# Kernel optimization log

Hardware: AMD Instinct MI355X
Metric: run time of the kernel (lower is better)

Reference implementation:

```python
import jax, jax.numpy as jnp
import numpy as np
from jax import lax
from jax.scipy.special import ndtr

EV = 6           # even context kernel size
K = 3            # num_mixtures
GROUPS = 3       # grouped 1x1 convs (grps=3 for clrchs<3)
SCALE_MIN = 0.11 # lower bound on mixture std
LP = 257         # 257 CDF sampling points (8-bit Y/RGB path)


def _cdf_pts():
    # cdf_sampling_pts__Y_RGB from __init__
    pts = jnp.linspace(-127.5, 128.5, LP) / 255.0
    pts = pts.at[0].set(-147.5 / 255.0).at[-1].set(148.5 / 255.0)
    return pts.astype(jnp.float32)


def _conv(x, w, b, groups=1):
    y = lax.conv_general_dilated(
        x, w, window_strides=(1, 1), padding='VALID',
        dimension_numbers=('NCHW', 'OIHW', 'NCHW'),
        feature_group_count=groups)
    return y + b[None, :, None, None]


def _forward_float(y_condition, W0, b0, W1, b1, W2, b2):
    # replicate pad: paddd0_00_11 = (Ev//2-1, Ev//2, Ev//2-1, Ev//2)
    y = jnp.pad(y_condition, ((0, 0), (0, 0), (EV // 2 - 1, EV // 2), (EV // 2 - 1, EV // 2)), mode='edge')
    h = jax.nn.relu(_conv(y, W0, b0, groups=1))        # [B, 192, H, W]
    h = jax.nn.relu(_conv(h, W1, b1, groups=GROUPS))   # [B, 192, H, W]
    p = _conv(h, W2, b2, groups=GROUPS)                # [B, 9, H, W] GMM params
    B, _, H, W = p.shape
    p = p.reshape(B, 3, K, H, W)                       # param-major: mu / raw_scale / raw_weight
    mu, sr, wr = p[:, 0], p[:, 1], p[:, 2]             # each [B, K, H, W]
    scale = jnp.maximum(jnp.exp(sr), SCALE_MIN)
    wts = jax.nn.softmax(wr, axis=1)                   # mixture weights over K
    t = _cdf_pts()                                     # [LP]
    z = (t - mu[..., None]) / scale[..., None]         # [B, K, H, W, LP]
    cdf = jnp.einsum('bkhw,bkhwl->bhwl', wts, ndtr(z)) # mixture CDF, [B, H, W, LP]
    return jnp.clip(cdf, 0.0, 1.0 - 1e-6)


def setup_inputs() -> dict:
    key = jax.random.key(0)
    ks = jax.random.split(key, 4)
    return {
        'y_condition': jax.random.uniform(ks[0], (1, 1, 256, 256), jnp.float32),
        'W0': jax.random.normal(ks[1], (192, 1, EV, EV), jnp.float32) * 0.05,
        'b0': jnp.zeros((192,), jnp.float32),
        'W1': jax.random.normal(ks[2], (192, 64, 1, 1), jnp.float32) * 0.05,
        'b1': jnp.zeros((192,), jnp.float32),
        'W2': jax.random.normal(ks[3], (9, 64, 1, 1), jnp.float32) * 0.05,
        'b2': jnp.zeros((9,), jnp.float32),
    }


def reference(y_condition, W0, b0, W1, b1, W2, b2):
    cdf_f = _forward_float(y_condition, W0, b0, W1, b1, W2, b2)
    # _convert_to_int_and_normalize with needs_normalization=True
    new_max = jnp.float32(2 ** 16 - (LP - 1))
    cdf_i = jnp.round(cdf_f * new_max).astype(jnp.int16)
    cdf_i = cdf_i + jnp.arange(LP, dtype=jnp.int16)
    return cdf_i
```

## Files before the change

### kernel.cpp

```cpp
#include <hip/hip_runtime.h>
#include <math.h>

#define LPTS 257
#define NPIX 65536
#define PPB  32
#define W1T_LD 68


__device__ __forceinline__ float xla_exp32(float x)
{
#pragma clang fp contract(off)
    x = fminf(x, 88.3762626647950f);
    x = fmaxf(x, -87.3365478515625f);
    const float m = floorf(fmaf(x, 1.44269504088896341f, 0.5f));
    float r = fmaf(m, -0.693359375f, x);
    r = fmaf(m, 2.12194440e-4f, r);
    const float r2 = r * r;
    float p = 1.9875691500e-4f;
    p = fmaf(p, r, 1.3981999507e-3f);
    p = fmaf(p, r, 8.3334519073e-3f);
    p = fmaf(p, r, 4.1665795894e-2f);
    p = fmaf(p, r, 1.6666665459e-1f);
    p = fmaf(p, r, 5.0000001201e-1f);
    float y = fmaf(p, r2, r) + 1.0f;
    const int e = (int)m;
    const float s = __int_as_float((e + 127) << 23);
    return y * s;
}

__device__ __forceinline__ float ieee_div(float n, float d)
{
    const float r0 = __builtin_amdgcn_rcpf(d);
    const float e  = fmaf(-d, r0, 1.0f);
    const float r1 = fmaf(e, r0, r0);
    const float q0 = n * r1;
    const float e1 = fmaf(-d, q0, n);
    const float q1 = fmaf(e1, r1, q0);
    const float e2 = fmaf(-d, q1, n);
    return fmaf(e2, r1, q1);
}

__device__ __forceinline__ float xla_erf32(float x)
{
#pragma clang fp contract(off)
    x = fminf(fmaxf(x, -4.0f), 4.0f);
    const float x2 = x * x;
    float pa = -2.72614225801306e-10f;
    pa = fmaf(pa, x2, 2.77068142495902e-08f);
    pa = fmaf(pa, x2, -2.10102402082508e-06f);
    pa = fmaf(pa, x2, -5.69250639462346e-05f);
    pa = fmaf(pa, x2, -7.34990630326855e-04f);
    pa = fmaf(pa, x2, -2.95459980854025e-03f);
    pa = fmaf(pa, x2, -1.60960333262415e-02f);
    float pb = -1.45660718464996e-05f;
    pb = fmaf(pb, x2, -2.13374055278905e-04f);
    pb = fmaf(pb, x2, -1.68282697438203e-03f);
    pb = fmaf(pb, x2, -7.37332916720468e-03f);
    pb = fmaf(pb, x2, -1.42647390514189e-02f);
    return ieee_div(x * pa, pb);
}

__device__ __forceinline__ float xla_erfc_ge1(float x)
{
#pragma clang fp contract(off)
    const float z = xla_exp32(-(x * x));
    const float q = 1.0f / x;
    const float y2 = q * q;
    float p;
    if (x < 2.0f) {
        p = 2.326819970068386e-02f;
        p = fmaf(p, y2, -1.387039388740657e-01f);
        p = fmaf(p, y2, 3.687424674597105e-01f);
        p = fmaf(p, y2, -5.824733027278666e-01f);
        p = fmaf(p, y2, 6.210004621745983e-01f);
        p = fmaf(p, y2, -4.944515323274145e-01f);
        p = fmaf(p, y2, 3.404879937665872e-01f);
        p = fmaf(p, y2, -2.741127028184656e-01f);
        p = fmaf(p, y2, 5.638259427386472e-01f);
    } else {
        p = -1.047766399936249e+01f;
        p = fmaf(p, y2, 1.297719955372516e+01f);
        p = fmaf(p, y2, -7.495518717768503e+00f);
        p = fmaf(p, y2, 2.921019019210786e+00f);
        p = fmaf(p, y2, -1.015265279202700e+00f);
        p = fmaf(p, y2, 4.218463358204948e-01f);
        p = fmaf(p, y2, -2.820767439740514e-01f);
        p = fmaf(p, y2, 5.641895067754075e-01f);
    }
    return z * q * p;
}

__device__ __forceinline__ void xla_ndtr3_y(
    float z0, float z1, float z2, float& o0, float& o1, float& o2)
{
#pragma clang fp contract(off)
    const float c = __uint_as_float(0x3f3504f3u);
    const float w0 = z0 * c, w1 = z1 * c, w2 = z2 * c;
    const float a0 = fabsf(w0), a1 = fabsf(w1), a2 = fabsf(w2);

    const float E0 = xla_erf32(w0);
    const float E1 = xla_erf32(w1);
    const float E2 = xla_erf32(w2);

    const float m0 = 1.0f - fabsf(E0);
    const float m1 = 1.0f - fabsf(E1);
    const float m2 = 1.0f - fabsf(E2);

    float y0 = (a0 < c) ? (1.0f + E0) : ((w0 > 0.0f) ? (2.0f - m0) : m0);
    float y1 = (a1 < c) ? (1.0f + E1) : ((w1 > 0.0f) ? (2.0f - m1) : m1);
    float y2 = (a2 < c) ? (1.0f + E2) : ((w2 > 0.0f) ? (2.0f - m2) : m2);

    const float amax = fmaxf(fmaxf(a0, a1), a2);
    if (__builtin_expect(__ballot(amax > 1.0f) != 0ull, 0)) {
        {
            const float ec = xla_erfc_ge1(a0);
            const float yc = (w0 > 0.0f) ? (2.0f - ec) : ec;
            y0 = (a0 > 1.0f) ? yc : y0;
        }
        {
            const float ec = xla_erfc_ge1(a1);
            const float yc = (w1 > 0.0f) ? (2.0f - ec) : ec;
            y1 = (a1 > 1.0f) ? yc : y1;
        }
        {
            const float ec = xla_erfc_ge1(a2);
            const float yc = (w2 > 0.0f) ? (2.0f - ec) : ec;
            y2 = (a2 > 1.0f) ? yc : y2;
        }
    }
    o0 = y0; o1 = y1; o2 = y2;
}

__device__ __forceinline__ float xla_ndtr32(float zf)
{
#pragma clang fp contract(off)
    const float c = __uint_as_float(0x3f3504f3u);
    const float w = zf * c;
    const float aw = fabsf(w);
    const float E = xla_erf32(w);
    const float e_mid = 1.0f - fabsf(E);
    float y = (aw < c) ? (1.0f + E)
                       : ((w > 0.0f) ? (2.0f - e_mid) : e_mid);
    if (__builtin_expect(__ballot(aw > 1.0f) != 0ull, 0)) {
        const float ec = xla_erfc_ge1(aw);
        const float yc = (w > 0.0f) ? (2.0f - ec) : ec;
        y = (aw > 1.0f) ? yc : y;
    }
    return 0.5f * y;
}

__device__ __forceinline__ int quantize(float cdf, int l)
{
    int r = (int)rintf(cdf * 65280.0f);
    r = r > 32767 ? 32767 : r;
    r = r < -32768 ? -32768 : r;
    return (int)((short)(r + l));
}

__global__ __launch_bounds__(256, 1) void entropy_params(
    const float* __restrict__ y,
    const float* __restrict__ W0, const float* __restrict__ b0,
    const float* __restrict__ W1, const float* __restrict__ b1,
    const float* __restrict__ W2, const float* __restrict__ b2,
    float* __restrict__ prm_g)
{
#pragma clang fp contract(off)
    __shared__ float tile[21][22];
    __shared__ __align__(16) float w0s[64 * 36];
    __shared__ __align__(16) float w1t[64 * W1T_LD];
    __shared__ __align__(16) float w2t[64 * 4];
    __shared__ __align__(16) float b0s[64];
    __shared__ __align__(16) float b1s[64];
    __shared__ float b2s[3];

    const int bx  = blockIdx.x & 15;
    const int by  = blockIdx.x >> 4;
    const int g   = blockIdx.y;
    const int tid = threadIdx.x;
    const int tx  = tid & 15;
    const int ty  = tid >> 4;

    {
        const float4* src = (const float4*)(W0 + g * 64 * 36);
        for (int i = tid; i < 576; i += 256) ((float4*)w0s)[i] = src[i];
    }
    {
        const float4* src = (const float4*)(W1 + g * 4096);
        for (int i4 = tid; i4 < 1024; i4 += 256) {
            const float4 v = src[i4];
            const int c2 = i4 >> 4;
            const int c1 = (i4 << 2) & 63;
            w1t[(c1 + 0) * W1T_LD + c2] = v.x;
            w1t[(c1 + 1) * W1T_LD + c2] = v.y;
            w1t[(c1 + 2) * W1T_LD + c2] = v.z;
            w1t[(c1 + 3) * W1T_LD + c2] = v.w;
        }
    }
    if (tid < 64) {
        const int c2 = tid;
        w2t[c2 * 4 + 0] = W2[(3 * g + 0) * 64 + c2];
        w2t[c2 * 4 + 1] = W2[(3 * g + 1) * 64 + c2];
        w2t[c2 * 4 + 2] = W2[(3 * g + 2) * 64 + c2];
        w2t[c2 * 4 + 3] = 0.0f;
    }
    {
        const float4* s0 = (const float4*)(b0 + g * 64);
        const float4* s1 = (const float4*)(b1 + g * 64);
        if (tid < 16)      ((float4*)b0s)[tid]      = s0[tid];
        else if (tid < 32) ((float4*)b1s)[tid - 16] = s1[tid - 16];
        if (tid < 3) b2s[tid] = b2[3 * g + tid];
    }
    for (int idx = tid; idx < 21 * 21; idx += 256) {
        const int r = idx / 21;
        const int c = idx - r * 21;
        int gy = by * 16 - 2 + r; gy = gy < 0 ? 0 : (gy > 255 ? 255 : gy);
        int gx = bx * 16 - 2 + c; gx = gx < 0 ? 0 : (gx > 255 ? 255 : gx);
        tile[r][c] = y[gy * 256 + gx];
    }
    __syncthreads();

    float patch[36];
#pragma unroll
    for (int i = 0; i < 6; ++i)
#pragma unroll
        for (int j = 0; j < 6; ++j)
            patch[i * 6 + j] = tile[ty + i][tx + j];

    float acc2[64];
#pragma unroll
    for (int j = 0; j < 64; ++j) acc2[j] = 0.0f;

#pragma unroll 2
    for (int c1 = 0; c1 < 64; ++c1) {
        const float4* w4 = (const float4*)(w0s + c1 * 36);
        float h = 0.0f;
#pragma unroll
        for (int q = 0; q < 9; ++q) {
            const float4 wv = w4[q];
            h = fmaf(wv.x, patch[4 * q + 0], h);
            h = fmaf(wv.y, patch[4 * q + 1], h);
            h = fmaf(wv.z, patch[4 * q + 2], h);
            h = fmaf(wv.w, patch[4 * q + 3], h);
        }
        h = fmaxf(h + b0s[c1], 0.0f);

        const float4* w1r = (const float4*)(w1t + c1 * W1T_LD);
#pragma unroll
        for (int qq = 0; qq < 16; ++qq) {
            const float4 wv = w1r[qq];
            acc2[4 * qq + 0] = fmaf(wv.x, h, acc2[4 * qq + 0]);
            acc2[4 * qq + 1] = fmaf(wv.y, h, acc2[4 * qq + 1]);
            acc2[4 * qq + 2] = fmaf(wv.z, h, acc2[4 * qq + 2]);
            acc2[4 * qq + 3] = fmaf(wv.w, h, acc2[4 * qq + 3]);
        }
    }

    float p0 = 0.0f, p1 = 0.0f, p2 = 0.0f;
#pragma unroll
    for (int c2 = 0; c2 < 64; ++c2) {
        const float h1 = fmaxf(acc2[c2] + b1s[c2], 0.0f);
        const float4 wv = *(const float4*)(w2t + c2 * 4);
        p0 = fmaf(wv.x, h1, p0);
        p1 = fmaf(wv.y, h1, p1);
        p2 = fmaf(wv.z, h1, p2);
    }
    p0 += b2s[0]; p1 += b2s[1]; p2 += b2s[2];

    const int pix = (by * 16 + ty) * 256 + bx * 16 + tx;

    if (g == 0) {
        prm_g[0 * NPIX + pix] = p0;
        prm_g[1 * NPIX + pix] = p1;
        prm_g[2 * NPIX + pix] = p2;
    } else if (g == 1) {
        const float s0 = fmaxf(xla_exp32(p0), 0.11f);
        const float s1 = fmaxf(xla_exp32(p1), 0.11f);
        const float s2 = fmaxf(xla_exp32(p2), 0.11f);
        prm_g[3 * NPIX + pix] = s0;
        prm_g[4 * NPIX + pix] = s1;
        prm_g[5 * NPIX + pix] = s2;
        prm_g[6 * NPIX + pix] = 1.0f / s0;
        prm_g[7 * NPIX + pix] = 1.0f / s1;
        prm_g[8 * NPIX + pix] = 1.0f / s2;
    } else {
        const float m  = fmaxf(fmaxf(p0, p1), p2);
        const float e0 = xla_exp32(p0 - m);
        const float e1 = xla_exp32(p1 - m);
        const float e2 = xla_exp32(p2 - m);
        const float s  = (e0 + e1) + e2;
        prm_g[ 9 * NPIX + pix] = 0.5f * (e0 / s);
        prm_g[10 * NPIX + pix] = 0.5f * (e1 / s);
        prm_g[11 * NPIX + pix] = 0.5f * (e2 / s);
    }
}

__global__ __launch_bounds__(256) void entropy_cdf(
    const float* __restrict__ prm_g,
    int* __restrict__ out)
{
#pragma clang fp contract(off)
    __shared__ __align__(16) float prm[PPB][12];

    const int base = blockIdx.x * PPB;
    const int tid  = threadIdx.x;

    for (int i = tid; i < 12 * PPB; i += 256) {
        const int j = i >> 5;
        const int p = i & 31;
        prm[p][j] = prm_g[j * NPIX + base + p];
    }
    __syncthreads();

    const float CLIP = (float)(1.0 - 1e-6);

    {
        const int l = tid;
        const float t32 = (l == 0)
            ? (float)(-147.5 / 255.0)
            : (float)((((double)l) - 127.5) / 255.0);
#pragma unroll 4
        for (int p = 0; p < PPB; ++p) {
            const float4 v0 = *(const float4*)&prm[p][0];
            const float4 v1 = *(const float4*)&prm[p][4];
            const float4 v2 = *(const float4*)&prm[p][8];

            const float x0 = t32 - v0.x;
            const float x1 = t32 - v0.y;
            const float x2 = t32 - v0.z;
            const float qa = x0 * v1.z;
            const float qb = x1 * v1.w;
            const float qc = x2 * v2.x;
            const float ra = fmaf(-v0.w, qa, x0);
            const float rb = fmaf(-v1.x, qb, x1);
            const float rc = fmaf(-v1.y, qc, x2);
            const float z0 = fmaf(ra, v1.z, qa);
            const float z1 = fmaf(rb, v1.w, qb);
            const float z2 = fmaf(rc, v2.x, qc);

            float y0, y1, y2;
            xla_ndtr3_y(z0, z1, z2, y0, y1, y2);

            float cdf = fmaf(v2.w, y2, fmaf(v2.z, y1, v2.y * y0));
            cdf = fminf(fmaxf(cdf, 0.0f), CLIP);

            out[(size_t)(base + p) * LPTS + l] = quantize(cdf, l);
        }
    }

    if (tid < PPB) {
        const int p = tid;
        const float t32 = (float)(148.5 / 255.0);
        const float4 v0 = *(const float4*)&prm[p][0];
        const float4 v1 = *(const float4*)&prm[p][4];
        const float4 v2 = *(const float4*)&prm[p][8];

        const float x0 = t32 - v0.x;
        const float x1 = t32 - v0.y;
        const float x2 = t32 - v0.z;
        const float qa = x0 * v1.z;
        const float qb = x1 * v1.w;
        const float qc = x2 * v2.x;
        const float ra = fmaf(-v0.w, qa, x0);
        const float rb = fmaf(-v1.x, qb, x1);
        const float rc = fmaf(-v1.y, qc, x2);
        const float z0 = fmaf(ra, v1.z, qa);
        const float z1 = fmaf(rb, v1.w, qb);
        const float z2 = fmaf(rc, v2.x, qc);

        float y0, y1, y2;
        xla_ndtr3_y(z0, z1, z2, y0, y1, y2);

        float cdf = fmaf(v2.w, y2, fmaf(v2.z, y1, v2.y * y0));
        cdf = fminf(fmaxf(cdf, 0.0f), CLIP);

        out[(size_t)(base + p) * LPTS + 256] = quantize(cdf, 256);
    }
}

__global__ __launch_bounds__(256) void entropy_fused(
    const float* __restrict__ y,
    const float* __restrict__ W0, const float* __restrict__ b0,
    const float* __restrict__ W1, const float* __restrict__ b1,
    const float* __restrict__ W2, const float* __restrict__ b2,
    int* __restrict__ out)
{
#pragma clang fp contract(off)

    __shared__ float tile[21][22];
    __shared__ float prm[9][257];

    const int bx  = blockIdx.x & 15;
    const int by  = blockIdx.x >> 4;
    const int tid = threadIdx.x;
    const int tx  = tid & 15;
    const int ty  = tid >> 4;

    for (int idx = tid; idx < 21 * 21; idx += 256) {
        const int r = idx / 21;
        const int c = idx - r * 21;
        int gy = by * 16 - 2 + r; gy = gy < 0 ? 0 : (gy > 255 ? 255 : gy);
        int gx = bx * 16 - 2 + c; gx = gx < 0 ? 0 : (gx > 255 ? 255 : gx);
        tile[r][c] = y[gy * 256 + gx];
    }
    __syncthreads();

    float patch[36];
#pragma unroll
    for (int i = 0; i < 6; ++i)
#pragma unroll
        for (int j = 0; j < 6; ++j)
            patch[i * 6 + j] = tile[ty + i][tx + j];

    for (int g = 0; g < 3; ++g) {
        float h0[64];
#pragma unroll
        for (int c = 0; c < 64; ++c) {
            float acc = 0.0f;
            const float* w = W0 + (g * 64 + c) * 36;
#pragma unroll
            for (int k = 0; k < 36; ++k)
                acc = fmaf(w[k], patch[k], acc);
            acc = acc + b0[g * 64 + c];
            h0[c] = fmaxf(acc, 0.0f);
        }

        float p0 = 0.0f, p1 = 0.0f, p2 = 0.0f;
#pragma unroll 2
        for (int c = 0; c < 64; ++c) {
            float acc = 0.0f;
            const float* w = W1 + (g * 64 + c) * 64;
#pragma unroll
            for (int j = 0; j < 64; ++j)
                acc = fmaf(w[j], h0[j], acc);
            acc = acc + b1[g * 64 + c];
            acc = fmaxf(acc, 0.0f);
            p0 = fmaf(W2[(3 * g + 0) * 64 + c], acc, p0);
            p1 = fmaf(W2[(3 * g + 1) * 64 + c], acc, p1);
            p2 = fmaf(W2[(3 * g + 2) * 64 + c], acc, p2);
        }
        p0 = p0 + b2[3 * g + 0];
        p1 = p1 + b2[3 * g + 1];
        p2 = p2 + b2[3 * g + 2];

        if (g == 0) {
            prm[0][tid] = p0; prm[1][tid] = p1; prm[2][tid] = p2;
        } else if (g == 1) {
            prm[3][tid] = fmaxf(xla_exp32(p0), 0.11f);
            prm[4][tid] = fmaxf(xla_exp32(p1), 0.11f);
            prm[5][tid] = fmaxf(xla_exp32(p2), 0.11f);
        } else {
            const float m  = fmaxf(fmaxf(p0, p1), p2);
            const float e0 = xla_exp32(p0 - m);
            const float e1 = xla_exp32(p1 - m);
            const float e2 = xla_exp32(p2 - m);
            const float s  = (e0 + e1) + e2;
            prm[6][tid] = e0 / s;
            prm[7][tid] = e1 / s;
            prm[8][tid] = e2 / s;
        }
    }
    __syncthreads();

    const int rowbase = (by * 16) * 256 + bx * 16;
    const float CLIP = (float)(1.0 - 1e-6);

    {
        const int l = tid;
        const float t32 = (l == 0)
            ? (float)(-147.5 / 255.0)
            : (float)((((double)l) - 127.5) / 255.0);
        for (int p = 0; p < 256; ++p) {
            const float mu0 = prm[0][p], mu1 = prm[1][p], mu2 = prm[2][p];
            const float sc0 = prm[3][p], sc1 = prm[4][p], sc2 = prm[5][p];
            const float w0  = prm[6][p], w1  = prm[7][p], w2  = prm[8][p];

            const float n0 = xla_ndtr32((t32 - mu0) / sc0);
            const float n1 = xla_ndtr32((t32 - mu1) / sc1);
            const float n2 = xla_ndtr32((t32 - mu2) / sc2);

            float cdf = fmaf(w2, n2, fmaf(w1, n1, w0 * n0));
            cdf = fminf(fmaxf(cdf, 0.0f), CLIP);

            const int pix = rowbase + (p >> 4) * 256 + (p & 15);
            out[(size_t)pix * LPTS + l] = quantize(cdf, l);
        }
    }

    {
        const int p = tid;
        const float t32 = (float)(148.5 / 255.0);
        const float mu0 = prm[0][p], mu1 = prm[1][p], mu2 = prm[2][p];
        const float sc0 = prm[3][p], sc1 = prm[4][p], sc2 = prm[5][p];
        const float w0  = prm[6][p], w1  = prm[7][p], w2  = prm[8][p];

        const float n0 = xla_ndtr32((t32 - mu0) / sc0);
        const float n1 = xla_ndtr32((t32 - mu1) / sc1);
        const float n2 = xla_ndtr32((t32 - mu2) / sc2);

        float cdf = fmaf(w2, n2, fmaf(w1, n1, w0 * n0));
        cdf = fminf(fmaxf(cdf, 0.0f), CLIP);

        const int pix = rowbase + (p >> 4) * 256 + (p & 15);
        out[(size_t)pix * LPTS + 256] = quantize(cdf, 256);
    }
}

extern "C" void kernel_launch(void* const* d_in, const int* in_sizes, int n_in,
                              void* d_out, int out_size, void* d_ws, size_t ws_size,
                              hipStream_t stream)
{
    const float* y  = (const float*)d_in[0];
    const float* W0 = (const float*)d_in[1];
    const float* b0 = (const float*)d_in[2];
    const float* W1 = (const float*)d_in[3];
    const float* b1 = (const float*)d_in[4];
    const float* W2 = (const float*)d_in[5];
    const float* b2 = (const float*)d_in[6];

    int* out = (int*)d_out;

    const size_t need = (size_t)12 * NPIX * sizeof(float);
    if (d_ws != nullptr && ws_size >= need) {
        float* prm_g = (float*)d_ws;
        entropy_params<<<dim3(256, 3), dim3(256), 0, stream>>>(
            y, W0, b0, W1, b1, W2, b2, prm_g);
        entropy_cdf<<<dim3(NPIX / PPB), dim3(256), 0, stream>>>(prm_g, out);
    } else {
        entropy_fused<<<dim3(256), dim3(256), 0, stream>>>(
            y, W0, b0, W1, b1, W2, b2, out);
    }
}
```

Before: 175.1 us.

## Split per-pixel channel work across four threads with shared-memory staging

The params kernel now gives each pixel four threads instead of one. Each thread computes 16 of the 64 channels for the conv0 and grouped conv1 stages, and the intermediate activations are staged in shared memory between stages. The block tile shrinks to 8x8 pixels, the grid grows fourfold, and the single-block occupancy hint is dropped. This cuts per-thread register pressure (the 64-float accumulator array is gone) and raises parallelism, at the cost of extra LDS traffic, three more barriers, and a final 9-output projection done by only one thread per pixel.

Result: slower. 180.2 us (+3.0%).

```diff
diff --git a/kernel.cpp b/kernel.cpp
--- a/kernel.cpp
+++ b/kernel.cpp
@@ -4,7 +4,7 @@
 #define LPTS 257
 #define NPIX 65536
 #define PPB  32
-#define W1T_LD 68
+#define SW   68
 
 
 __device__ __forceinline__ float xla_exp32(float x)
@@ -157,7 +157,7 @@
     return (int)((short)(r + l));
 }
 
-__global__ __launch_bounds__(256, 1) void entropy_params(
+__global__ __launch_bounds__(256) void entropy_params(
     const float* __restrict__ y,
     const float* __restrict__ W0, const float* __restrict__ b0,
     const float* __restrict__ W1, const float* __restrict__ b1,
@@ -165,23 +165,26 @@
     float* __restrict__ prm_g)
 {
 #pragma clang fp contract(off)
-    __shared__ float tile[21][22];
+    __shared__ __align__(16) float tile[13][16];
     __shared__ __align__(16) float w0s[64 * 36];
-    __shared__ __align__(16) float w1t[64 * W1T_LD];
+    __shared__ __align__(16) float w1s[64 * SW];
     __shared__ __align__(16) float w2t[64 * 4];
     __shared__ __align__(16) float b0s[64];
     __shared__ __align__(16) float b1s[64];
     __shared__ float b2s[3];
-
-    const int bx  = blockIdx.x & 15;
-    const int by  = blockIdx.x >> 4;
+    __shared__ __align__(16) float h0s[64 * SW];
+
+    const int bx  = blockIdx.x & 31;
+    const int by  = blockIdx.x >> 5;
     const int g   = blockIdx.y;
     const int tid = threadIdx.x;
-    const int tx  = tid & 15;
-    const int ty  = tid >> 4;
+    const int p   = tid >> 2;
+    const int t   = tid & 3;
+    const int py  = p >> 3;
+    const int px  = p & 7;
 
     {
-        const float4* src = (const float4*)(W0 + g * 64 * 36);
+        const float4* src = (const float4*)(W0 + g * 2304);
         for (int i = tid; i < 576; i += 256) ((float4*)w0s)[i] = src[i];
     }
     {
@@ -189,33 +192,28 @@
         for (int i4 = tid; i4 < 1024; i4 += 256) {
             const float4 v = src[i4];
             const int c2 = i4 >> 4;
-            const int c1 = (i4 << 2) & 63;
-            w1t[(c1 + 0) * W1T_LD + c2] = v.x;
-            w1t[(c1 + 1) * W1T_LD + c2] = v.y;
-            w1t[(c1 + 2) * W1T_LD + c2] = v.z;
-            w1t[(c1 + 3) * W1T_LD + c2] = v.w;
+            const int k4 = (i4 & 15) << 2;
+            *(float4*)&w1s[c2 * SW + k4] = v;
         }
     }
     if (tid < 64) {
-        const int c2 = tid;
-        w2t[c2 * 4 + 0] = W2[(3 * g + 0) * 64 + c2];
-        w2t[c2 * 4 + 1] = W2[(3 * g + 1) * 64 + c2];
-        w2t[c2 * 4 + 2] = W2[(3 * g + 2) * 64 + c2];
-        w2t[c2 * 4 + 3] = 0.0f;
-    }
-    {
-        const float4* s0 = (const float4*)(b0 + g * 64);
-        const float4* s1 = (const float4*)(b1 + g * 64);
-        if (tid < 16)      ((float4*)b0s)[tid]      = s0[tid];
-        else if (tid < 32) ((float4*)b1s)[tid - 16] = s1[tid - 16];
-        if (tid < 3) b2s[tid] = b2[3 * g + tid];
-    }
-    for (int idx = tid; idx < 21 * 21; idx += 256) {
-        const int r = idx / 21;
-        const int c = idx - r * 21;
-        int gy = by * 16 - 2 + r; gy = gy < 0 ? 0 : (gy > 255 ? 255 : gy);
-        int gx = bx * 16 - 2 + c; gx = gx < 0 ? 0 : (gx > 255 ? 255 : gx);
-        tile[r][c] = y[gy * 256 + gx];
+        w2t[tid * 4 + 0] = W2[(3 * g + 0) * 64 + tid];
+        w2t[tid * 4 + 1] = W2[(3 * g + 1) * 64 + tid];
+        w2t[tid * 4 + 2] = W2[(3 * g + 2) * 64 + tid];
+        w2t[tid * 4 + 3] = 0.0f;
+    } else if (tid < 128) {
+        b0s[tid - 64] = b0[g * 64 + (tid - 64)];
+    } else if (tid < 192) {
+        b1s[tid - 128] = b1[g * 64 + (tid - 128)];
+    }
+    if (tid < 3) b2s[tid] = b2[3 * g + tid];
+
+    if (tid < 169) {
+        const int rr = tid / 13;
+        const int cc = tid - rr * 13;
+        int gy = by * 8 - 2 + rr;  gy = gy < 0 ? 0 : (gy > 255 ? 255 : gy);
+        int gx = bx * 8 - 2 + cc;  gx = gx < 0 ? 0 : (gx > 255 ? 255 : gx);
+        tile[rr][cc] = y[gy * 256 + gx];
     }
     __syncthreads();
 
@@ -224,73 +222,100 @@
     for (int i = 0; i < 6; ++i)
 #pragma unroll
         for (int j = 0; j < 6; ++j)
-            patch[i * 6 + j] = tile[ty + i][tx + j];
-
-    float acc2[64];
-#pragma unroll
-    for (int j = 0; j < 64; ++j) acc2[j] = 0.0f;
-
-#pragma unroll 2
-    for (int c1 = 0; c1 < 64; ++c1) {
-        const float4* w4 = (const float4*)(w0s + c1 * 36);
-        float h = 0.0f;
-#pragma unroll
-        for (int q = 0; q < 9; ++q) {
-            const float4 wv = w4[q];
-            h = fmaf(wv.x, patch[4 * q + 0], h);
-            h = fmaf(wv.y, patch[4 * q + 1], h);
-            h = fmaf(wv.z, patch[4 * q + 2], h);
-            h = fmaf(wv.w, patch[4 * q + 3], h);
-        }
-        h = fmaxf(h + b0s[c1], 0.0f);
-
-        const float4* w1r = (const float4*)(w1t + c1 * W1T_LD);
-#pragma unroll
-        for (int qq = 0; qq < 16; ++qq) {
-            const float4 wv = w1r[qq];
-            acc2[4 * qq + 0] = fmaf(wv.x, h, acc2[4 * qq + 0]);
-            acc2[4 * qq + 1] = fmaf(wv.y, h, acc2[4 * qq + 1]);
-            acc2[4 * qq + 2] = fmaf(wv.z, h, acc2[4 * qq + 2]);
-            acc2[4 * qq + 3] = fmaf(wv.w, h, acc2[4 * qq + 3]);
-        }
-    }
-
-    float p0 = 0.0f, p1 = 0.0f, p2 = 0.0f;
-#pragma unroll
-    for (int c2 = 0; c2 < 64; ++c2) {
-        const float h1 = fmaxf(acc2[c2] + b1s[c2], 0.0f);
-        const float4 wv = *(const float4*)(w2t + c2 * 4);
-        p0 = fmaf(wv.x, h1, p0);
-        p1 = fmaf(wv.y, h1, p1);
-        p2 = fmaf(wv.z, h1, p2);
-    }
-    p0 += b2s[0]; p1 += b2s[1]; p2 += b2s[2];
-
-    const int pix = (by * 16 + ty) * 256 + bx * 16 + tx;
-
-    if (g == 0) {
-        prm_g[0 * NPIX + pix] = p0;
-        prm_g[1 * NPIX + pix] = p1;
-        prm_g[2 * NPIX + pix] = p2;
-    } else if (g == 1) {
-        const float s0 = fmaxf(xla_exp32(p0), 0.11f);
-        const float s1 = fmaxf(xla_exp32(p1), 0.11f);
-        const float s2 = fmaxf(xla_exp32(p2), 0.11f);
-        prm_g[3 * NPIX + pix] = s0;
-        prm_g[4 * NPIX + pix] = s1;
-        prm_g[5 * NPIX + pix] = s2;
-        prm_g[6 * NPIX + pix] = 1.0f / s0;
-        prm_g[7 * NPIX + pix] = 1.0f / s1;
-        prm_g[8 * NPIX + pix] = 1.0f / s2;
-    } else {
-        const float m  = fmaxf(fmaxf(p0, p1), p2);
-        const float e0 = xla_exp32(p0 - m);
-        const float e1 = xla_exp32(p1 - m);
-        const float e2 = xla_exp32(p2 - m);
-        const float s  = (e0 + e1) + e2;
-        prm_g[ 9 * NPIX + pix] = 0.5f * (e0 / s);
-        prm_g[10 * NPIX + pix] = 0.5f * (e1 / s);
-        prm_g[11 * NPIX + pix] = 0.5f * (e2 / s);
+            patch[i * 6 + j] = tile[py + i][px + j];
+
+    float h[16];
+#pragma unroll
+    for (int j = 0; j < 16; ++j) h[j] = 0.0f;
+#pragma unroll
+    for (int q = 0; q < 9; ++q) {
+        const float pk0 = patch[4 * q + 0];
+        const float pk1 = patch[4 * q + 1];
+        const float pk2 = patch[4 * q + 2];
+        const float pk3 = patch[4 * q + 3];
+#pragma unroll
+        for (int j = 0; j < 16; ++j) {
+            const int c1 = t + 4 * j;
+            const float4 wv = *(const float4*)&w0s[c1 * 36 + 4 * q];
+            h[j] = fmaf(wv.x, pk0, h[j]);
+            h[j] = fmaf(wv.y, pk1, h[j]);
+            h[j] = fmaf(wv.z, pk2, h[j]);
+            h[j] = fmaf(wv.w, pk3, h[j]);
+        }
+    }
+#pragma unroll
+    for (int j = 0; j < 16; ++j) {
+        const int c1 = t + 4 * j;
+        h0s[p * SW + c1] = fmaxf(h[j] + b0s[c1], 0.0f);
+    }
+    __syncthreads();
+
+    float a2[16];
+#pragma unroll
+    for (int j = 0; j < 16; ++j) a2[j] = 0.0f;
+#pragma unroll
+    for (int k = 0; k < 16; ++k) {
+        const float4 hv = *(const float4*)&h0s[p * SW + 4 * k];
+#pragma unroll
+        for (int j = 0; j < 16; ++j) {
+            const int c2 = t + 4 * j;
+            const float4 wv = *(const float4*)&w1s[c2 * SW + 4 * k];
+            a2[j] = fmaf(wv.x, hv.x, a2[j]);
+            a2[j] = fmaf(wv.y, hv.y, a2[j]);
+            a2[j] = fmaf(wv.z, hv.z, a2[j]);
+            a2[j] = fmaf(wv.w, hv.w, a2[j]);
+        }
+    }
+    __syncthreads();
+#pragma unroll
+    for (int j = 0; j < 16; ++j) {
+        const int c2 = t + 4 * j;
+        h0s[p * SW + c2] = fmaxf(a2[j] + b1s[c2], 0.0f);
+    }
+    __syncthreads();
+
+    if (t == 0) {
+        float p0 = 0.0f, p1 = 0.0f, p2 = 0.0f;
+#pragma unroll
+        for (int k = 0; k < 16; ++k) {
+            const float4 hv = *(const float4*)&h0s[p * SW + 4 * k];
+            const float hva[4] = {hv.x, hv.y, hv.z, hv.w};
+#pragma unroll
+            for (int i = 0; i < 4; ++i) {
+                const float4 wv = *(const float4*)&w2t[(4 * k + i) * 4];
+                p0 = fmaf(wv.x, hva[i], p0);
+                p1 = fmaf(wv.y, hva[i], p1);
+                p2 = fmaf(wv.z, hva[i], p2);
+            }
+        }
+        p0 += b2s[0]; p1 += b2s[1]; p2 += b2s[2];
+
+        const int pix = (by * 8 + py) * 256 + bx * 8 + px;
+
+        if (g == 0) {
+            prm_g[0 * NPIX + pix] = p0;
+            prm_g[1 * NPIX + pix] = p1;
+            prm_g[2 * NPIX + pix] = p2;
+        } else if (g == 1) {
+            const float s0 = fmaxf(xla_exp32(p0), 0.11f);
+            const float s1 = fmaxf(xla_exp32(p1), 0.11f);
+            const float s2 = fmaxf(xla_exp32(p2), 0.11f);
+            prm_g[3 * NPIX + pix] = s0;
+            prm_g[4 * NPIX + pix] = s1;
+            prm_g[5 * NPIX + pix] = s2;
+            prm_g[6 * NPIX + pix] = 1.0f / s0;
+            prm_g[7 * NPIX + pix] = 1.0f / s1;
+            prm_g[8 * NPIX + pix] = 1.0f / s2;
+        } else {
+            const float m  = fmaxf(fmaxf(p0, p1), p2);
+            const float e0 = xla_exp32(p0 - m);
+            const float e1 = xla_exp32(p1 - m);
+            const float e2 = xla_exp32(p2 - m);
+            const float s  = (e0 + e1) + e2;
+            prm_g[ 9 * NPIX + pix] = 0.5f * (e0 / s);
+            prm_g[10 * NPIX + pix] = 0.5f * (e1 / s);
+            prm_g[11 * NPIX + pix] = 0.5f * (e2 / s);
+        }
     }
 }
 
@@ -522,7 +547,7 @@
     const size_t need = (size_t)12 * NPIX * sizeof(float);
     if (d_ws != nullptr && ws_size >= need) {
         float* prm_g = (float*)d_ws;
-        entropy_params<<<dim3(256, 3), dim3(256), 0, stream>>>(
+        entropy_params<<<dim3(1024, 3), dim3(256), 0, stream>>>(
             y, W0, b0, W1, b1, W2, b2, prm_g);
         entropy_cdf<<<dim3(NPIX / PPB), dim3(256), 0, stream>>>(prm_g, out);
     } else {
```
